# Optimization experiments

Hardware: AMD Instinct MI355X
Metric: run time of the kernel (lower is better)

## Reference

```python
import jax, jax.numpy as jnp
import numpy as np

NEG_BIG = 1e13  # matches the torch module's (mask-1)*1e13 additive mask


def setup_inputs() -> dict:
    key = jax.random.key(0)
    k1, k2, k3, k4 = jax.random.split(key, 4)
    B, Lq, Lk, D = 32, 1024, 1024, 1024  # D = 2*hidden = 2*embedding
    query = jax.random.normal(k1, (B, Lq, D), dtype=jnp.float32)
    key_t = jax.random.normal(k2, (B, Lk, D), dtype=jnp.float32)
    key_mask = jax.random.randint(k3, (B, Lk), 0, 2).astype(jnp.float32)
    # Linear(hidden*2 -> embedding*2): weight [out, in] torch convention
    W = jax.random.normal(k4, (D, D), dtype=jnp.float32) * (1.0 / np.sqrt(D))
    b = jnp.zeros((D,), dtype=jnp.float32)
    return {"query": query, "key": key_t, "key_mask": key_mask, "W": W, "b": b}


def reference(query, key, key_mask, W, b):
    # query_emb: Dropout (identity at eval) -> Linear -> ReLU
    query_feat = jax.nn.relu(jnp.einsum("bqd,ed->bqe", query, W) + b)  # [B,Lq,D]
    # bmm with multiplicatively masked key
    masked_key = key * key_mask[:, :, None]                             # [B,Lk,D]
    score = jnp.einsum("bqd,bkd->bqk", query_feat, masked_key)          # [B,Lq,Lk]
    # masked_softmax: score*mask + (mask-1)*1e13, softmax over last dim
    m = key_mask[:, None, :]                                            # [B,1,Lk]
    attn = jax.nn.softmax(score * m + (m - 1.0) * NEG_BIG, axis=-1)     # [B,Lq,Lk]
    # weighted sum over the UNmasked key (as in the original module)
    return jnp.einsum("bqk,bkd->bqd", attn, key)                        # [B,Lq,D]
```

## Files before the change

kernel.cpp:

```cpp
#include <hip/hip_runtime.h>
#include <hip/hip_bf16.h>


typedef __attribute__((ext_vector_type(4))) float f32x4;
typedef __attribute__((ext_vector_type(8))) short s16x8;

#define MFMA16(a, b, c) __builtin_amdgcn_mfma_f32_16x16x32_bf16((a), (b), (c), 0, 0, 0)

__device__ __forceinline__ unsigned short f2bf(float x) {
  unsigned u = __builtin_bit_cast(unsigned, x);
  return (unsigned short)((u + 0x7FFFu + ((u >> 16) & 1u)) >> 16);
}
__device__ __forceinline__ float bf2f(unsigned short h) {
  return __builtin_bit_cast(float, ((unsigned)h) << 16);
}
__device__ __forceinline__ int swz(int row, int col) {
  return (row * 64 + col) ^ ((row & 7) << 3);
}
__device__ __forceinline__ void cvt8(const float* __restrict__ s, s16x8& h8, s16x8& l8) {
  f32x4 a = *(const f32x4*)s;
  f32x4 b = *(const f32x4*)(s + 4);
#pragma unroll
  for (int i = 0; i < 8; i++) {
    float v = (i < 4) ? a[i] : b[i - 4];
    unsigned short hu = f2bf(v);
    unsigned short lu = f2bf(v - bf2f(hu));
    h8[i] = (short)hu;
    l8[i] = (short)lu;
  }
}
__device__ __forceinline__ void gld16(const void* g, void* lds) {
  __builtin_amdgcn_global_load_lds((const __attribute__((address_space(1))) unsigned int*)g,
                                   (__attribute__((address_space(3))) unsigned int*)lds, 16, 0, 0);
}

#define OFF_KHI 0ULL
#define OFF_KLO 67108864ULL
#define OFF_KHIT 134217728ULL
#define OFF_QHI 201326592ULL
#define OFF_QLO 268435456ULL
#define OFF_WHI 335544320ULL
#define OFF_WLO 337641472ULL
#define WS_TIER_A 339738624ULL
#define QA_LO 33554432ULL

__global__ __launch_bounds__(256) void k_cvt_pair(const float* __restrict__ src,
                                                  unsigned short* __restrict__ hi,
                                                  unsigned short* __restrict__ lo, int n8) {
  int i = blockIdx.x * 256 + threadIdx.x;
  if (i >= n8) return;
  s16x8 h, l;
  cvt8(src + (size_t)i * 8, h, l);
  *(s16x8*)(hi + (size_t)i * 8) = h;
  *(s16x8*)(lo + (size_t)i * 8) = l;
}

__global__ __launch_bounds__(256) void k_cvt_k(const float* __restrict__ K,
                                               unsigned short* __restrict__ Khi,
                                               unsigned short* __restrict__ Klo,
                                               unsigned short* __restrict__ KhiT) {
  __shared__ unsigned T[64 * 65];
  const int t = threadIdx.x;
  const int db0 = blockIdx.x * 64, kb0 = blockIdx.y * 64, b = blockIdx.z;
  const size_t base = (size_t)b * 1024 * 1024;
#pragma unroll
  for (int i = 0; i < 2; i++) {
    const int r = (t >> 3) + i * 32, c0 = (t & 7) * 8;
    s16x8 h, l;
    cvt8(K + base + (size_t)(kb0 + r) * 1024 + db0 + c0, h, l);
    *(s16x8*)(Khi + base + (size_t)(kb0 + r) * 1024 + db0 + c0) = h;
    *(s16x8*)(Klo + base + (size_t)(kb0 + r) * 1024 + db0 + c0) = l;
#pragma unroll
    for (int j = 0; j < 8; j++)
      T[r * 65 + c0 + j] = ((unsigned)(unsigned short)h[j] << 16) | (unsigned short)l[j];
  }
  __syncthreads();
#pragma unroll
  for (int i = 0; i < 2; i++) {
    const int rd = (t >> 3) + i * 32, ck0 = (t & 7) * 8;
    s16x8 h;
#pragma unroll
    for (int j = 0; j < 8; j++) h[j] = (short)(unsigned short)(T[(ck0 + j) * 65 + rd] >> 16);
    *(s16x8*)(KhiT + base + (size_t)(db0 + rd) * 1024 + kb0 + ck0) = h;
  }
}

__global__ __launch_bounds__(256, 2) void k_qf2(const unsigned short* __restrict__ Qhi,
                                                const unsigned short* __restrict__ Qlo,
                                                const unsigned short* __restrict__ Whi,
                                                const unsigned short* __restrict__ Wlo,
                                                const float* __restrict__ bias,
                                                float* __restrict__ outp) {
  __shared__ __align__(16) unsigned short Ah[128 * 64], Al[128 * 64], Bh[128 * 64], Bl[128 * 64];
  const int t = threadIdx.x;
  const int i = blockIdx.x + blockIdx.y * 256;
  const int x = i & 7, j = i >> 3;
  const int n0 = (j & 7) * 128;
  const int m0 = (x * 32 + (j >> 3)) * 128;
  const int w = t >> 6, l = t & 63, wm = w >> 1, wn = w & 1, g = l >> 4, ln = l & 15;
  const int lrow = l >> 3, lc8 = (l & 7) * 8;
  const f32x4 fz = {0.f, 0.f, 0.f, 0.f};
  f32x4 acc[4][4];
#pragma unroll
  for (int a = 0; a < 4; a++)
#pragma unroll
    for (int bq = 0; bq < 4; bq++) acc[a][bq] = fz;
#pragma unroll 1
  for (int k0 = 0; k0 < 1024; k0 += 64) {
#pragma unroll
    for (int jj = 0; jj < 4; jj++) {
      const int ch = w * 4 + jj;
      const int row = ch * 8 + lrow;
      const int sc = lc8 ^ (lrow << 3);
      gld16(Qhi + (size_t)(m0 + row) * 1024 + k0 + sc, &Ah[ch * 512]);
      gld16(Qlo + (size_t)(m0 + row) * 1024 + k0 + sc, &Al[ch * 512]);
      gld16(Whi + (size_t)(n0 + row) * 1024 + k0 + sc, &Bh[ch * 512]);
      gld16(Wlo + (size_t)(n0 + row) * 1024 + k0 + sc, &Bl[ch * 512]);
    }
    __syncthreads();
#pragma unroll
    for (int ks = 0; ks < 2; ks++) {
      const int kc = ks * 32 + g * 8;
      s16x8 ah[4], al[4], bh[4], bl[4];
#pragma unroll
      for (int mf = 0; mf < 4; mf++) {
        const int row = wm * 64 + mf * 16 + ln;
        const int idx = row * 64 + (kc ^ ((row & 7) << 3));
        ah[mf] = *(const s16x8*)&Ah[idx];
        al[mf] = *(const s16x8*)&Al[idx];
      }
#pragma unroll
      for (int nf = 0; nf < 4; nf++) {
        const int row = wn * 64 + nf * 16 + ln;
        const int idx = row * 64 + (kc ^ ((row & 7) << 3));
        bh[nf] = *(const s16x8*)&Bh[idx];
        bl[nf] = *(const s16x8*)&Bl[idx];
      }
#pragma unroll
      for (int mf = 0; mf < 4; mf++)
#pragma unroll
        for (int nf = 0; nf < 4; nf++) {
          acc[mf][nf] = MFMA16(ah[mf], bh[nf], acc[mf][nf]);
          acc[mf][nf] = MFMA16(ah[mf], bl[nf], acc[mf][nf]);
          acc[mf][nf] = MFMA16(al[mf], bh[nf], acc[mf][nf]);
        }
    }
    __syncthreads();
  }
  unsigned short* qA = (unsigned short*)outp;
#pragma unroll
  for (int nf = 0; nf < 4; nf++) {
    const int c = n0 + wn * 64 + nf * 16 + ln;
    const float bv = bias[c];
    const int kchunk = c >> 5, lhib = ((c >> 3) & 3) << 4, jj = c & 7;
#pragma unroll
    for (int mf = 0; mf < 4; mf++)
#pragma unroll
      for (int r = 0; r < 4; r++) {
        const int R = m0 + wm * 64 + mf * 16 + g * 4 + r;
        float v = acc[mf][nf][r] + bv;
        v = v > 0.f ? v : 0.f;
        unsigned short h = f2bf(v);
        const size_t fo = (((size_t)(R >> 4) * 32 + kchunk) * 64 + ((R & 15) + lhib)) * 8 + jj;
        qA[fo] = h;
        qA[QA_LO + fo] = f2bf(v - bf2f(h));
      }
  }
}

__global__ __launch_bounds__(512, 2) void k_attn2(const unsigned short* __restrict__ Khi,
                                                  const unsigned short* __restrict__ Klo,
                                                  const float* __restrict__ mask,
                                                  const unsigned short* __restrict__ qA,
                                                  unsigned short* __restrict__ attnw) {
  __shared__ __align__(16) unsigned short kbuf[2][2][128 * 64];
  __shared__ float mask_s[1024];
  __shared__ float red[4][64];
  const int t = threadIdx.x;
  const int i = blockIdx.y * 16 + blockIdx.x;
  const int x = i & 7, jj = i >> 3;
  const int b = x * 4 + (jj >> 4), qt = jj & 15;
  const int q0 = qt * 64;
  const int w = t >> 6, l = t & 63, wm = w >> 2, wn = w & 3, g = l >> 4, ln = l & 15;
  const int lrow = l >> 3, lc8 = (l & 7) * 8, sc = lc8 ^ (lrow << 3);
  for (int ii = t; ii < 1024; ii += 512) mask_s[ii] = mask[b * 1024 + ii];
  const f32x4 fz = {0.f, 0.f, 0.f, 0.f};
  f32x4 acc[8][2][2];
#pragma unroll
  for (int kt = 0; kt < 8; kt++)
#pragma unroll
    for (int mf = 0; mf < 2; mf++)
#pragma unroll
      for (int nf = 0; nf < 2; nf++) acc[kt][mf][nf] = fz;
  const size_t kbase = (size_t)b * 1024 * 1024;
  const int qblk0 = (b * 1024 + q0) >> 4;

  auto stageK = [&](int buf, int kt, int dc) {
#pragma unroll
    for (int jj2 = 0; jj2 < 2; jj2++) {
      const int ch = w * 2 + jj2;
      const int row = ch * 8 + lrow;
      const size_t go = kbase + (size_t)(kt * 128 + row) * 1024 + dc * 64 + sc;
      gld16(Khi + go, &kbuf[buf][0][ch * 512]);
      gld16(Klo + go, &kbuf[buf][1][ch * 512]);
    }
  };

  stageK(0, 0, 0);
  __syncthreads();
#pragma unroll 1
  for (int dc = 0; dc < 16; dc++) {
    s16x8 qh[2][2], ql[2][2];
#pragma unroll
    for (int mf = 0; mf < 2; mf++) {
      const int qb = qblk0 + wm * 2 + mf;
#pragma unroll
      for (int ks = 0; ks < 2; ks++) {
        const size_t fo = (((size_t)qb * 32 + dc * 2 + ks) * 64 + l) * 8;
        qh[mf][ks] = *(const s16x8*)(qA + fo);
        ql[mf][ks] = *(const s16x8*)(qA + QA_LO + fo);
      }
    }
#pragma unroll
    for (int kt = 0; kt < 8; kt++) {
      const int snum = dc * 8 + kt;
      if (snum == 127) {
        asm volatile("s_waitcnt vmcnt(0)" ::: "memory");
      } else if (kt == 0) {
        asm volatile("s_waitcnt vmcnt(8)" ::: "memory");
      } else {
        asm volatile("s_waitcnt vmcnt(4)" ::: "memory");
      }
      __builtin_amdgcn_s_barrier();
      __builtin_amdgcn_sched_barrier(0);
      if (snum < 127) {
        const int nkt = (kt + 1) & 7;
        const int ndc = (kt == 7) ? dc + 1 : dc;
        stageK((snum + 1) & 1, nkt, ndc);
      }
      const int cur = snum & 1;
#pragma unroll
      for (int ks = 0; ks < 2; ks++) {
        const int kc = ks * 32 + g * 8;
        s16x8 bh[2], bl[2];
#pragma unroll
        for (int nf = 0; nf < 2; nf++) {
          const int row = wn * 32 + nf * 16 + ln;
          const int idx = row * 64 + (kc ^ ((row & 7) << 3));
          bh[nf] = *(const s16x8*)&kbuf[cur][0][idx];
          bl[nf] = *(const s16x8*)&kbuf[cur][1][idx];
        }
#pragma unroll
        for (int mf = 0; mf < 2; mf++)
#pragma unroll
          for (int nf = 0; nf < 2; nf++) {
            acc[kt][mf][nf] = MFMA16(qh[mf][ks], bh[nf], acc[kt][mf][nf]);
            acc[kt][mf][nf] = MFMA16(qh[mf][ks], bl[nf], acc[kt][mf][nf]);
            acc[kt][mf][nf] = MFMA16(ql[mf][ks], bh[nf], acc[kt][mf][nf]);
          }
      }
    }
  }
  __syncthreads();
  float rmax[2][4];
#pragma unroll
  for (int mf = 0; mf < 2; mf++)
#pragma unroll
    for (int r = 0; r < 4; r++) rmax[mf][r] = -1e30f;
#pragma unroll
  for (int kt = 0; kt < 8; kt++)
#pragma unroll
    for (int nf = 0; nf < 2; nf++) {
      const int k = kt * 128 + wn * 32 + nf * 16 + ln;
      const bool mk = mask_s[k] != 0.f;
#pragma unroll
      for (int mf = 0; mf < 2; mf++)
#pragma unroll
        for (int r = 0; r < 4; r++)
          if (mk) rmax[mf][r] = fmaxf(rmax[mf][r], acc[kt][mf][nf][r]);
    }
#pragma unroll
  for (int off = 1; off < 16; off <<= 1)
#pragma unroll
    for (int mf = 0; mf < 2; mf++)
#pragma unroll
      for (int r = 0; r < 4; r++) rmax[mf][r] = fmaxf(rmax[mf][r], __shfl_xor(rmax[mf][r], off));
  if (ln == 0) {
#pragma unroll
    for (int mf = 0; mf < 2; mf++)
#pragma unroll
      for (int r = 0; r < 4; r++) red[wn][wm * 32 + mf * 16 + g * 4 + r] = rmax[mf][r];
  }
  __syncthreads();
#pragma unroll
  for (int mf = 0; mf < 2; mf++)
#pragma unroll
    for (int r = 0; r < 4; r++) {
      const int row = wm * 32 + mf * 16 + g * 4 + r;
      rmax[mf][r] = fmaxf(fmaxf(red[0][row], red[1][row]), fmaxf(red[2][row], red[3][row]));
    }
  __syncthreads();
  float rsum[2][4];
#pragma unroll
  for (int mf = 0; mf < 2; mf++)
#pragma unroll
    for (int r = 0; r < 4; r++) rsum[mf][r] = 0.f;
#pragma unroll
  for (int kt = 0; kt < 8; kt++)
#pragma unroll
    for (int nf = 0; nf < 2; nf++) {
      const int k = kt * 128 + wn * 32 + nf * 16 + ln;
      const bool mk = mask_s[k] != 0.f;
#pragma unroll
      for (int mf = 0; mf < 2; mf++)
#pragma unroll
        for (int r = 0; r < 4; r++)
          if (mk) rsum[mf][r] += __expf(acc[kt][mf][nf][r] - rmax[mf][r]);
    }
#pragma unroll
  for (int off = 1; off < 16; off <<= 1)
#pragma unroll
    for (int mf = 0; mf < 2; mf++)
#pragma unroll
      for (int r = 0; r < 4; r++) rsum[mf][r] += __shfl_xor(rsum[mf][r], off);
  if (ln == 0) {
#pragma unroll
    for (int mf = 0; mf < 2; mf++)
#pragma unroll
      for (int r = 0; r < 4; r++) red[wn][wm * 32 + mf * 16 + g * 4 + r] = rsum[mf][r];
  }
  __syncthreads();
  float rinv[2][4];
#pragma unroll
  for (int mf = 0; mf < 2; mf++)
#pragma unroll
    for (int r = 0; r < 4; r++) {
      const int row = wm * 32 + mf * 16 + g * 4 + r;
      rinv[mf][r] = 1.f / (red[0][row] + red[1][row] + red[2][row] + red[3][row]);
    }
#pragma unroll
  for (int kt = 0; kt < 8; kt++)
#pragma unroll
    for (int nf = 0; nf < 2; nf++) {
      const int k = kt * 128 + wn * 32 + nf * 16 + ln;
      const bool mk = mask_s[k] != 0.f;
#pragma unroll
      for (int mf = 0; mf < 2; mf++)
#pragma unroll
        for (int r = 0; r < 4; r++) {
          const int q = q0 + wm * 32 + mf * 16 + g * 4 + r;
          float p = mk ? __expf(acc[kt][mf][nf][r] - rmax[mf][r]) * rinv[mf][r] : 0.f;
          attnw[(size_t)(b * 1024 + q) * 1024 + k] = f2bf(p);
        }
    }
}

__global__ __launch_bounds__(512, 2) void k_pv2(const unsigned short* __restrict__ KhiT,
                                                const unsigned short* __restrict__ attnw,
                                                float* __restrict__ dout) {
  __shared__ __align__(16) unsigned short P[128 * 64];
  __shared__ __align__(16) unsigned short KT[512 * 64];
  const int t = threadIdx.x;
  const int i = blockIdx.y * 8 + blockIdx.x;
  const int x = i & 7, jj = i >> 3;
  const int b = x * 4 + (jj >> 3), qt = jj & 7;
  const int q0 = qt * 128, d0 = blockIdx.z * 512;
  const int w = t >> 6, l = t & 63, wm = w >> 2, wd = w & 3, g = l >> 4, ln = l & 15;
  const int lrow = l >> 3, lc8 = (l & 7) * 8, sc = lc8 ^ (lrow << 3);
  const f32x4 fz = {0.f, 0.f, 0.f, 0.f};
  f32x4 acc[4][8];
#pragma unroll
  for (int a = 0; a < 4; a++)
#pragma unroll
    for (int bq = 0; bq < 8; bq++) acc[a][bq] = fz;
  const size_t kbase = (size_t)b * 1024 * 1024;
#pragma unroll 1
  for (int k0 = 0; k0 < 1024; k0 += 64) {
#pragma unroll
    for (int jj2 = 0; jj2 < 2; jj2++) {
      const int ch = w * 2 + jj2;
      const int row = ch * 8 + lrow;
      gld16(attnw + (size_t)(b * 1024 + q0 + row) * 1024 + k0 + sc, &P[ch * 512]);
    }
#pragma unroll
    for (int jj2 = 0; jj2 < 8; jj2++) {
      const int ch = w * 8 + jj2;
      const int row = ch * 8 + lrow;
      gld16(KhiT + kbase + (size_t)(d0 + row) * 1024 + k0 + sc, &KT[ch * 512]);
    }
    __syncthreads();
#pragma unroll
    for (int ks = 0; ks < 2; ks++) {
      const int kc = ks * 32 + g * 8;
      s16x8 a[4], bb[8];
#pragma unroll
      for (int mf = 0; mf < 4; mf++) {
        const int row = wm * 64 + mf * 16 + ln;
        a[mf] = *(const s16x8*)&P[row * 64 + (kc ^ ((row & 7) << 3))];
      }
#pragma unroll
      for (int nf = 0; nf < 8; nf++) {
        const int row = wd * 128 + nf * 16 + ln;
        bb[nf] = *(const s16x8*)&KT[row * 64 + (kc ^ ((row & 7) << 3))];
      }
#pragma unroll
      for (int mf = 0; mf < 4; mf++)
#pragma unroll
        for (int nf = 0; nf < 8; nf++) acc[mf][nf] = MFMA16(a[mf], bb[nf], acc[mf][nf]);
    }
    __syncthreads();
  }
#pragma unroll
  for (int mf = 0; mf < 4; mf++)
#pragma unroll
    for (int nf = 0; nf < 8; nf++)
#pragma unroll
      for (int r = 0; r < 4; r++) {
        const int q = q0 + wm * 64 + mf * 16 + g * 4 + r;
        const int d = d0 + wd * 128 + nf * 16 + ln;
        dout[(size_t)(b * 1024 + q) * 1024 + d] = acc[mf][nf][r];
      }
}

__global__ __launch_bounds__(256, 2) void k_qf(const float* __restrict__ Q,
                                               const float* __restrict__ W,
                                               const float* __restrict__ bias,
                                               float* __restrict__ qf) {
  __shared__ __align__(16) short Ah[128 * 64], Al[128 * 64], Bh[128 * 64], Bl[128 * 64];
  const int t = threadIdx.x;
  const int m0 = blockIdx.x * 128, n0 = blockIdx.y * 128;
  const int w = t >> 6, l = t & 63, wm = w >> 1, wn = w & 1, g = l >> 4, ln = l & 15;
  const f32x4 fz = {0.f, 0.f, 0.f, 0.f};
  f32x4 acc[4][4];
#pragma unroll
  for (int a = 0; a < 4; a++)
#pragma unroll
    for (int bq = 0; bq < 4; bq++) acc[a][bq] = fz;
  const int srow = t >> 1, scol = (t & 1) * 32;
#pragma unroll 1
  for (int k0 = 0; k0 < 1024; k0 += 64) {
    const float* sa = Q + (size_t)(m0 + srow) * 1024 + k0 + scol;
    const float* sb = W + (size_t)(n0 + srow) * 1024 + k0 + scol;
#pragma unroll
    for (int c = 0; c < 32; c += 8) {
      s16x8 h, lo;
      cvt8(sa + c, h, lo);
      int si = swz(srow, scol + c);
      *(s16x8*)&Ah[si] = h;
      *(s16x8*)&Al[si] = lo;
    }
#pragma unroll
    for (int c = 0; c < 32; c += 8) {
      s16x8 h, lo;
      cvt8(sb + c, h, lo);
      int si = swz(srow, scol + c);
      *(s16x8*)&Bh[si] = h;
      *(s16x8*)&Bl[si] = lo;
    }
    __syncthreads();
#pragma unroll
    for (int ks = 0; ks < 2; ks++) {
      const int kc = ks * 32 + g * 8;
      s16x8 ah[4], al[4], bh[4], bl[4];
#pragma unroll
      for (int mf = 0; mf < 4; mf++) {
        int si = swz(wm * 64 + mf * 16 + ln, kc);
        ah[mf] = *(s16x8*)&Ah[si];
        al[mf] = *(s16x8*)&Al[si];
      }
#pragma unroll
      for (int nf = 0; nf < 4; nf++) {
        int si = swz(wn * 64 + nf * 16 + ln, kc);
        bh[nf] = *(s16x8*)&Bh[si];
        bl[nf] = *(s16x8*)&Bl[si];
      }
#pragma unroll
      for (int mf = 0; mf < 4; mf++)
#pragma unroll
        for (int nf = 0; nf < 4; nf++) {
          acc[mf][nf] = MFMA16(ah[mf], bh[nf], acc[mf][nf]);
          acc[mf][nf] = MFMA16(ah[mf], bl[nf], acc[mf][nf]);
          acc[mf][nf] = MFMA16(al[mf], bh[nf], acc[mf][nf]);
        }
    }
    __syncthreads();
  }
#pragma unroll
  for (int nf = 0; nf < 4; nf++) {
    const int col = n0 + wn * 64 + nf * 16 + ln;
    const float bv = bias[col];
#pragma unroll
    for (int mf = 0; mf < 4; mf++)
#pragma unroll
      for (int r = 0; r < 4; r++) {
        const int row = m0 + wm * 64 + mf * 16 + g * 4 + r;
        float v = acc[mf][nf][r] + bv;
        qf[(size_t)row * 1024 + col] = v > 0.f ? v : 0.f;
      }
  }
}

__global__ __launch_bounds__(512, 2) void k_attn(const float* __restrict__ Key,
                                                 const float* __restrict__ mask,
                                                 float* __restrict__ dout) {
  __shared__ __align__(16) short qh[64 * 64], qlo[64 * 64], kh[128 * 64], klo[128 * 64];
  __shared__ float mask_s[1024];
  __shared__ float red[4][64];
  const int t = threadIdx.x;
  const int qt = blockIdx.x, b = blockIdx.y;
  const int q0 = qt * 64;
  const int w = t >> 6, l = t & 63, wm = w >> 2, wn = w & 3, g = l >> 4, ln = l & 15;
  for (int i = t; i < 1024; i += 512) mask_s[i] = mask[b * 1024 + i];
  const f32x4 fz = {0.f, 0.f, 0.f, 0.f};
  f32x4 acc[8][2][2];
#pragma unroll
  for (int kt = 0; kt < 8; kt++)
#pragma unroll
    for (int mf = 0; mf < 2; mf++)
#pragma unroll
      for (int nf = 0; nf < 2; nf++) acc[kt][mf][nf] = fz;
  const float* qfb = dout + (size_t)(b * 1024 + q0) * 1024;
  const float* kb = Key + (size_t)b * 1024 * 1024;
  const int qrow = t >> 3, qcol = (t & 7) * 8;
  const int krow = t >> 2, kcol0 = (t & 3) * 16;
#pragma unroll 1
  for (int dc = 0; dc < 16; dc++) {
    {
      s16x8 h, lo;
      cvt8(qfb + (size_t)qrow * 1024 + dc * 64 + qcol, h, lo);
      int si = swz(qrow, qcol);
      *(s16x8*)&qh[si] = h;
      *(s16x8*)&qlo[si] = lo;
    }
#pragma unroll
    for (int kt = 0; kt < 8; kt++) {
      {
        const float* s = kb + (size_t)(kt * 128 + krow) * 1024 + dc * 64 + kcol0;
        s16x8 h, lo;
        cvt8(s, h, lo);
        int si = swz(krow, kcol0);
        *(s16x8*)&kh[si] = h;
        *(s16x8*)&klo[si] = lo;
        cvt8(s + 8, h, lo);
        si = swz(krow, kcol0 + 8);
        *(s16x8*)&kh[si] = h;
        *(s16x8*)&klo[si] = lo;
      }
      __syncthreads();
#pragma unroll
      for (int ks = 0; ks < 2; ks++) {
        const int kc = ks * 32 + g * 8;
        s16x8 ah[2], al2[2], bh[2], bl[2];
#pragma unroll
        for (int mf = 0; mf < 2; mf++) {
          int si = swz(wm * 32 + mf * 16 + ln, kc);
          ah[mf] = *(s16x8*)&qh[si];
          al2[mf] = *(s16x8*)&qlo[si];
        }
#pragma unroll
        for (int nf = 0; nf < 2; nf++) {
          int si = swz(wn * 32 + nf * 16 + ln, kc);
          bh[nf] = *(s16x8*)&kh[si];
          bl[nf] = *(s16x8*)&klo[si];
        }
#pragma unroll
        for (int mf = 0; mf < 2; mf++)
#pragma unroll
          for (int nf = 0; nf < 2; nf++) {
            acc[kt][mf][nf] = MFMA16(ah[mf], bh[nf], acc[kt][mf][nf]);
            acc[kt][mf][nf] = MFMA16(ah[mf], bl[nf], acc[kt][mf][nf]);
            acc[kt][mf][nf] = MFMA16(al2[mf], bh[nf], acc[kt][mf][nf]);
          }
      }
      __syncthreads();
    }
  }
  float rmax[2][4];
#pragma unroll
  for (int mf = 0; mf < 2; mf++)
#pragma unroll
    for (int r = 0; r < 4; r++) rmax[mf][r] = -1e30f;
#pragma unroll
  for (int kt = 0; kt < 8; kt++)
#pragma unroll
    for (int nf = 0; nf < 2; nf++) {
      const int k = kt * 128 + wn * 32 + nf * 16 + ln;
      const bool mk = mask_s[k] != 0.f;
#pragma unroll
      for (int mf = 0; mf < 2; mf++)
#pragma unroll
        for (int r = 0; r < 4; r++)
          if (mk) rmax[mf][r] = fmaxf(rmax[mf][r], acc[kt][mf][nf][r]);
    }
#pragma unroll
  for (int off = 1; off < 16; off <<= 1)
#pragma unroll
    for (int mf = 0; mf < 2; mf++)
#pragma unroll
      for (int r = 0; r < 4; r++) rmax[mf][r] = fmaxf(rmax[mf][r], __shfl_xor(rmax[mf][r], off));
  if (ln == 0) {
#pragma unroll
    for (int mf = 0; mf < 2; mf++)
#pragma unroll
      for (int r = 0; r < 4; r++) red[wn][wm * 32 + mf * 16 + g * 4 + r] = rmax[mf][r];
  }
  __syncthreads();
#pragma unroll
  for (int mf = 0; mf < 2; mf++)
#pragma unroll
    for (int r = 0; r < 4; r++) {
      const int row = wm * 32 + mf * 16 + g * 4 + r;
      rmax[mf][r] = fmaxf(fmaxf(red[0][row], red[1][row]), fmaxf(red[2][row], red[3][row]));
    }
  __syncthreads();
  float rsum[2][4];
#pragma unroll
  for (int mf = 0; mf < 2; mf++)
#pragma unroll
    for (int r = 0; r < 4; r++) rsum[mf][r] = 0.f;
#pragma unroll
  for (int kt = 0; kt < 8; kt++)
#pragma unroll
    for (int nf = 0; nf < 2; nf++) {
      const int k = kt * 128 + wn * 32 + nf * 16 + ln;
      const bool mk = mask_s[k] != 0.f;
#pragma unroll
      for (int mf = 0; mf < 2; mf++)
#pragma unroll
        for (int r = 0; r < 4; r++)
          if (mk) rsum[mf][r] += __expf(acc[kt][mf][nf][r] - rmax[mf][r]);
    }
#pragma unroll
  for (int off = 1; off < 16; off <<= 1)
#pragma unroll
    for (int mf = 0; mf < 2; mf++)
#pragma unroll
      for (int r = 0; r < 4; r++) rsum[mf][r] += __shfl_xor(rsum[mf][r], off);
  if (ln == 0) {
#pragma unroll
    for (int mf = 0; mf < 2; mf++)
#pragma unroll
      for (int r = 0; r < 4; r++) red[wn][wm * 32 + mf * 16 + g * 4 + r] = rsum[mf][r];
  }
  __syncthreads();
  float rinv[2][4];
#pragma unroll
  for (int mf = 0; mf < 2; mf++)
#pragma unroll
    for (int r = 0; r < 4; r++) {
      const int row = wm * 32 + mf * 16 + g * 4 + r;
      rinv[mf][r] = 1.f / (red[0][row] + red[1][row] + red[2][row] + red[3][row]);
    }
  char* oc = (char*)dout;
#pragma unroll
  for (int kt = 0; kt < 8; kt++)
#pragma unroll
    for (int nf = 0; nf < 2; nf++) {
      const int k = kt * 128 + wn * 32 + nf * 16 + ln;
      const bool mk = mask_s[k] != 0.f;
#pragma unroll
      for (int mf = 0; mf < 2; mf++)
#pragma unroll
        for (int r = 0; r < 4; r++) {
          const int q = q0 + wm * 32 + mf * 16 + g * 4 + r;
          float p = mk ? __expf(acc[kt][mf][nf][r] - rmax[mf][r]) * rinv[mf][r] : 0.f;
          *(unsigned short*)(oc + (size_t)(b * 1024 + q) * 4096 + 2048 + k * 2) = f2bf(p);
        }
    }
}

__global__ __launch_bounds__(512, 2) void k_pv(const float* __restrict__ Key,
                                               float* __restrict__ dout, const int dh) {
  __shared__ __align__(16) short P[128 * 64];
  __shared__ __align__(16) short KT[512 * 64];
  const int t = threadIdx.x;
  const int qt = blockIdx.x, b = blockIdx.y;
  const int q0 = qt * 128, d0 = dh * 512;
  const int w = t >> 6, l = t & 63, wm = w >> 2, wd = w & 3, g = l >> 4, ln = l & 15;
  const f32x4 fz = {0.f, 0.f, 0.f, 0.f};
  f32x4 acc[4][8];
#pragma unroll
  for (int a = 0; a < 4; a++)
#pragma unroll
    for (int bq = 0; bq < 8; bq++) acc[a][bq] = fz;
  const char* ab = (const char*)dout;
  const int prow = t >> 2, pc0 = (t & 3) * 16;
#pragma unroll 1
  for (int k0 = 0; k0 < 1024; k0 += 64) {
    {
      const unsigned short* s =
          (const unsigned short*)(ab + (size_t)(b * 1024 + q0 + prow) * 4096 + 2048) + k0 + pc0;
      s16x8 p0 = *(const s16x8*)s, p1 = *(const s16x8*)(s + 8);
      *(s16x8*)&P[swz(prow, pc0)] = p0;
      *(s16x8*)&P[swz(prow, pc0 + 8)] = p1;
    }
    {
      const float* ksrc = Key + (size_t)b * 1024 * 1024 + (size_t)k0 * 1024 + d0 + t;
#pragma unroll
      for (int kg = 0; kg < 8; kg++) {
        s16x8 h;
#pragma unroll
        for (int jx = 0; jx < 8; jx++) h[jx] = (short)f2bf(ksrc[(size_t)(kg * 8 + jx) * 1024]);
        *(s16x8*)&KT[swz(t, kg * 8)] = h;
      }
    }
    __syncthreads();
#pragma unroll
    for (int ks = 0; ks < 2; ks++) {
      const int kc = ks * 32 + g * 8;
      s16x8 a[4], bb[8];
#pragma unroll
      for (int mf = 0; mf < 4; mf++) a[mf] = *(s16x8*)&P[swz(wm * 64 + mf * 16 + ln, kc)];
#pragma unroll
      for (int nf = 0; nf < 8; nf++) bb[nf] = *(s16x8*)&KT[swz(wd * 128 + nf * 16 + ln, kc)];
#pragma unroll
      for (int mf = 0; mf < 4; mf++)
#pragma unroll
        for (int nf = 0; nf < 8; nf++) acc[mf][nf] = MFMA16(a[mf], bb[nf], acc[mf][nf]);
    }
    __syncthreads();
  }
#pragma unroll
  for (int mf = 0; mf < 4; mf++)
#pragma unroll
    for (int nf = 0; nf < 8; nf++)
#pragma unroll
      for (int r = 0; r < 4; r++) {
        const int q = q0 + wm * 64 + mf * 16 + g * 4 + r;
        const int d = d0 + wd * 128 + nf * 16 + ln;
        dout[(size_t)(b * 1024 + q) * 1024 + d] = acc[mf][nf][r];
      }
}

extern "C" void kernel_launch(void* const* d_in, const int* in_sizes, int n_in,
                              void* d_out, int out_size, void* d_ws, size_t ws_size,
                              hipStream_t stream) {
  const float* Q = (const float*)d_in[0];
  const float* K = (const float*)d_in[1];
  const float* M = (const float*)d_in[2];
  const float* W = (const float*)d_in[3];
  const float* bias = (const float*)d_in[4];
  float* out = (float*)d_out;
  char* wsb = (char*)d_ws;
  (void)in_sizes; (void)n_in; (void)out_size;

  if (ws_size >= WS_TIER_A) {
    unsigned short* Khi = (unsigned short*)(wsb + OFF_KHI);
    unsigned short* Klo = (unsigned short*)(wsb + OFF_KLO);
    unsigned short* KhiT = (unsigned short*)(wsb + OFF_KHIT);
    unsigned short* Qhi = (unsigned short*)(wsb + OFF_QHI);
    unsigned short* Qlo = (unsigned short*)(wsb + OFF_QLO);
    unsigned short* Whi = (unsigned short*)(wsb + OFF_WHI);
    unsigned short* Wlo = (unsigned short*)(wsb + OFF_WLO);
    unsigned short* attnw = Qhi;
    k_cvt_k<<<dim3(16, 16, 32), 256, 0, stream>>>(K, Khi, Klo, KhiT);
    k_cvt_pair<<<16384, 256, 0, stream>>>(Q, Qhi, Qlo, 4194304);
    k_cvt_pair<<<512, 256, 0, stream>>>(W, Whi, Wlo, 131072);
    k_qf2<<<dim3(256, 8), 256, 0, stream>>>(Qhi, Qlo, Whi, Wlo, bias, out);
    k_attn2<<<dim3(16, 32), 512, 0, stream>>>(Khi, Klo, M, (const unsigned short*)out, attnw);
    k_pv2<<<dim3(8, 32, 2), 512, 0, stream>>>(KhiT, attnw, out);
  } else {
    k_qf<<<dim3(256, 8), 256, 0, stream>>>(Q, W, bias, out);
    k_attn<<<dim3(16, 32), 512, 0, stream>>>(K, M, out);
    k_pv<<<dim3(8, 32), 512, 0, stream>>>(K, out, 0);
    k_pv<<<dim3(8, 32), 512, 0, stream>>>(K, out, 1);
  }
}
```

Measured before the change: 727.7 us.

## Double-buffer PV kernel LDS staging, raise MFMA priority, merge Q/W conversions

The P·V kernel now double-buffers its attention-weight and transposed-K tiles in LDS. It prefetches the next k-slice with global_load_lds while computing the current one and drops the second __syncthreads per iteration. This doubles LDS use, so launch bounds drop to one block per SM. Both the score and PV inner MFMA loops are wrapped in s_setprio to favour math waves. The separate Q and W fp32-to-bf16 hi/lo conversion launches are merged into one kernel to save a launch.

```diff
diff --git a/kernel.cpp b/kernel.cpp
--- a/kernel.cpp
+++ b/kernel.cpp
@@ -44,15 +44,26 @@
 #define WS_TIER_A 339738624ULL
 #define QA_LO 33554432ULL
 
-__global__ __launch_bounds__(256) void k_cvt_pair(const float* __restrict__ src,
-                                                  unsigned short* __restrict__ hi,
-                                                  unsigned short* __restrict__ lo, int n8) {
+__global__ __launch_bounds__(256) void k_cvt_qw(const float* __restrict__ Q,
+                                                unsigned short* __restrict__ Qhi,
+                                                unsigned short* __restrict__ Qlo,
+                                                const float* __restrict__ W,
+                                                unsigned short* __restrict__ Whi,
+                                                unsigned short* __restrict__ Wlo) {
   int i = blockIdx.x * 256 + threadIdx.x;
-  if (i >= n8) return;
   s16x8 h, l;
-  cvt8(src + (size_t)i * 8, h, l);
-  *(s16x8*)(hi + (size_t)i * 8) = h;
-  *(s16x8*)(lo + (size_t)i * 8) = l;
+  if (i < 4194304) {
+    cvt8(Q + (size_t)i * 8, h, l);
+    *(s16x8*)(Qhi + (size_t)i * 8) = h;
+    *(s16x8*)(Qlo + (size_t)i * 8) = l;
+  } else {
+    int j = i - 4194304;
+    if (j < 131072) {
+      cvt8(W + (size_t)j * 8, h, l);
+      *(s16x8*)(Whi + (size_t)j * 8) = h;
+      *(s16x8*)(Wlo + (size_t)j * 8) = l;
+    }
+  }
 }
 
 __global__ __launch_bounds__(256) void k_cvt_k(const float* __restrict__ K,
@@ -239,6 +250,7 @@
         stageK((snum + 1) & 1, nkt, ndc);
       }
       const int cur = snum & 1;
+      __builtin_amdgcn_s_setprio(1);
 #pragma unroll
       for (int ks = 0; ks < 2; ks++) {
         const int kc = ks * 32 + g * 8;
@@ -259,6 +271,7 @@
             acc[kt][mf][nf] = MFMA16(ql[mf][ks], bh[nf], acc[kt][mf][nf]);
           }
       }
+      __builtin_amdgcn_s_setprio(0);
     }
   }
   __syncthreads();
@@ -355,11 +368,11 @@
     }
 }
 
-__global__ __launch_bounds__(512, 2) void k_pv2(const unsigned short* __restrict__ KhiT,
+__global__ __launch_bounds__(512, 1) void k_pv2(const unsigned short* __restrict__ KhiT,
                                                 const unsigned short* __restrict__ attnw,
                                                 float* __restrict__ dout) {
-  __shared__ __align__(16) unsigned short P[128 * 64];
-  __shared__ __align__(16) unsigned short KT[512 * 64];
+  __shared__ __align__(16) unsigned short Pb[2][128 * 64];
+  __shared__ __align__(16) unsigned short KTb[2][512 * 64];
   const int t = threadIdx.x;
   const int i = blockIdx.y * 8 + blockIdx.x;
   const int x = i & 7, jj = i >> 3;
@@ -374,21 +387,37 @@
 #pragma unroll
     for (int bq = 0; bq < 8; bq++) acc[a][bq] = fz;
   const size_t kbase = (size_t)b * 1024 * 1024;
-#pragma unroll 1
-  for (int k0 = 0; k0 < 1024; k0 += 64) {
+
+  auto stageP = [&](int buf, int k0) {
 #pragma unroll
     for (int jj2 = 0; jj2 < 2; jj2++) {
       const int ch = w * 2 + jj2;
       const int row = ch * 8 + lrow;
-      gld16(attnw + (size_t)(b * 1024 + q0 + row) * 1024 + k0 + sc, &P[ch * 512]);
-    }
+      gld16(attnw + (size_t)(b * 1024 + q0 + row) * 1024 + k0 + sc, &Pb[buf][ch * 512]);
+    }
+  };
+  auto stageKT = [&](int buf, int k0) {
 #pragma unroll
     for (int jj2 = 0; jj2 < 8; jj2++) {
       const int ch = w * 8 + jj2;
       const int row = ch * 8 + lrow;
-      gld16(KhiT + kbase + (size_t)(d0 + row) * 1024 + k0 + sc, &KT[ch * 512]);
-    }
-    __syncthreads();
+      gld16(KhiT + kbase + (size_t)(d0 + row) * 1024 + k0 + sc, &KTb[buf][ch * 512]);
+    }
+  };
+
+  stageP(0, 0);
+  stageKT(0, 0);
+#pragma unroll 1
+  for (int s = 0; s < 16; s++) {
+    asm volatile("s_waitcnt vmcnt(0)" ::: "memory");
+    __builtin_amdgcn_s_barrier();
+    __builtin_amdgcn_sched_barrier(0);
+    if (s < 15) {
+      stageP((s + 1) & 1, (s + 1) * 64);
+      stageKT((s + 1) & 1, (s + 1) * 64);
+    }
+    const int cur = s & 1;
+    __builtin_amdgcn_s_setprio(1);
 #pragma unroll
     for (int ks = 0; ks < 2; ks++) {
       const int kc = ks * 32 + g * 8;
@@ -396,19 +425,19 @@
 #pragma unroll
       for (int mf = 0; mf < 4; mf++) {
         const int row = wm * 64 + mf * 16 + ln;
-        a[mf] = *(const s16x8*)&P[row * 64 + (kc ^ ((row & 7) << 3))];
+        a[mf] = *(const s16x8*)&Pb[cur][row * 64 + (kc ^ ((row & 7) << 3))];
       }
 #pragma unroll
       for (int nf = 0; nf < 8; nf++) {
         const int row = wd * 128 + nf * 16 + ln;
-        bb[nf] = *(const s16x8*)&KT[row * 64 + (kc ^ ((row & 7) << 3))];
+        bb[nf] = *(const s16x8*)&KTb[cur][row * 64 + (kc ^ ((row & 7) << 3))];
       }
 #pragma unroll
       for (int mf = 0; mf < 4; mf++)
 #pragma unroll
         for (int nf = 0; nf < 8; nf++) acc[mf][nf] = MFMA16(a[mf], bb[nf], acc[mf][nf]);
     }
-    __syncthreads();
+    __builtin_amdgcn_s_setprio(0);
   }
 #pragma unroll
   for (int mf = 0; mf < 4; mf++)
@@ -754,8 +783,7 @@
     unsigned short* Wlo = (unsigned short*)(wsb + OFF_WLO);
     unsigned short* attnw = Qhi;
     k_cvt_k<<<dim3(16, 16, 32), 256, 0, stream>>>(K, Khi, Klo, KhiT);
-    k_cvt_pair<<<16384, 256, 0, stream>>>(Q, Qhi, Qlo, 4194304);
-    k_cvt_pair<<<512, 256, 0, stream>>>(W, Whi, Wlo, 131072);
+    k_cvt_qw<<<16896, 256, 0, stream>>>(Q, Qhi, Qlo, W, Whi, Wlo);
     k_qf2<<<dim3(256, 8), 256, 0, stream>>>(Qhi, Qlo, Whi, Wlo, bias, out);
     k_attn2<<<dim3(16, 32), 512, 0, stream>>>(Khi, Klo, M, (const unsigned short*)out, attnw);
     k_pv2<<<dim3(8, 32, 2), 512, 0, stream>>>(KhiT, attnw, out);
```

After: 722.3 us. No clear change (-0.7%).
